# Kernel optimization log

Hardware: AMD Instinct MI355X
Metric: run time of the kernel (lower is better)

## Reference

```python
import jax, jax.numpy as jnp
import numpy as np

IN_FEATURES = 4096
OUT_FEATURES = 4096
BLOCKSIZE = 64
FP4_CODEBOOK = np.array([0.0, 0.0052, 0.6667, 1.0, 0.3333, 0.5, 0.1667, 0.25,
                         0.0, -0.0052, -0.6667, -1.0, -0.3333, -0.5, -0.1667, -0.25],
                        dtype=np.float32)


def setup_inputs() -> dict:
    key = jax.random.key(0)
    k1, k2, k3, k4 = jax.random.split(key, 4)
    n_elements = OUT_FEATURES * IN_FEATURES
    n_blocks = n_elements // BLOCKSIZE
    x = jax.random.normal(k1, (4, 2048, IN_FEATURES), dtype=jnp.float32)
    weight_packed = jax.random.randint(k2, (n_elements // 2,), 0, 256, dtype=jnp.int32)
    scale = jax.random.uniform(k3, (n_blocks,), dtype=jnp.float32)
    bias = jax.random.normal(k4, (OUT_FEATURES,), dtype=jnp.float32)
    return {"x": x, "weight_packed": weight_packed, "scale": scale, "bias": bias}


def reference(x, weight_packed, scale, bias):
    codebook = jnp.asarray(FP4_CODEBOOK, dtype=x.dtype)
    # Unpack two 4-bit indices per byte: high nibble first, then low nibble.
    high = (weight_packed >> 4) & 15
    low = weight_packed & 15
    indices = jnp.stack([high, low], axis=1).reshape(-1)  # [n_elements]
    # LUT dequant + per-block scale broadcast.
    deq = codebook[indices].reshape(-1, BLOCKSIZE) * scale[:, None]  # [n_blocks, blocksize]
    weight = deq.reshape(OUT_FEATURES, IN_FEATURES)
    # F.linear(x, W, b) = x @ W.T + b
    return jnp.einsum('bsi,oi->bso', x, weight) + bias
```

## Files before the change

kernel.cpp:

```cpp
#include <hip/hip_runtime.h>
#include <stdint.h>
#include <stddef.h>

#define IN_F 4096
#define OUT_F 4096
#define M_TOT 8192

#define BM 128
#define BN 128
#define BK 64

#define BM2 256
#define BN2 256
#define BK2 64
#define NT2 (IN_F / BK2)

typedef __attribute__((ext_vector_type(8))) short short8;
typedef __attribute__((ext_vector_type(4))) float f32x4;
typedef __attribute__((ext_vector_type(4))) float float4v;
typedef __attribute__((ext_vector_type(4))) unsigned short u16x4;
typedef __attribute__((ext_vector_type(8))) unsigned short u16x8;
typedef unsigned short u16;

__constant__ float c_lut[16] = {
  0.0f, 0.0052f, 0.6667f, 1.0f, 0.3333f, 0.5f, 0.1667f, 0.25f,
  0.0f, -0.0052f, -0.6667f, -1.0f, -0.3333f, -0.5f, -0.1667f, -0.25f
};

__device__ __forceinline__ u16 f2bf(float f) {
  unsigned int x = __float_as_uint(f);
  x += 0x7fffu + ((x >> 16) & 1u);
  return (u16)(x >> 16);
}

__device__ __forceinline__ void gload_lds16(const u16* g, u16* lds) {
  __builtin_amdgcn_global_load_lds(
      (const __attribute__((address_space(1))) unsigned int*)g,
      (__attribute__((address_space(3))) unsigned int*)lds, 16, 0, 0);
}

#define BARRIER() do { asm volatile("" ::: "memory"); \
                       __builtin_amdgcn_s_barrier();  \
                       asm volatile("" ::: "memory"); } while (0)
#define LGKM0() asm volatile("s_waitcnt lgkmcnt(0)" ::: "memory")

__global__ __launch_bounds__(256) void k_convert_x(const float* __restrict__ x,
                                                   u16* __restrict__ a) {
  const int n8 = (M_TOT * IN_F) / 8;
  const int stride = gridDim.x * blockDim.x;
  for (int t = blockIdx.x * blockDim.x + threadIdx.x; t < n8; t += stride) {
    float4v f0 = ((const float4v*)x)[2 * t];
    float4v f1 = ((const float4v*)x)[2 * t + 1];
    u16x8 o;
    o[0] = f2bf(f0.x); o[1] = f2bf(f0.y); o[2] = f2bf(f0.z); o[3] = f2bf(f0.w);
    o[4] = f2bf(f1.x); o[5] = f2bf(f1.y); o[6] = f2bf(f1.z); o[7] = f2bf(f1.w);
    ((u16x8*)a)[t] = o;
  }
}

__global__ __launch_bounds__(256) void k_dequant_w(const int* __restrict__ wp,
                                                   const float* __restrict__ scale,
                                                   u16* __restrict__ b) {
  __shared__ float lut[16];
  if (threadIdx.x < 16) lut[threadIdx.x] = c_lut[threadIdx.x];
  __syncthreads();
  const int ng = (OUT_F * IN_F / 2) / 4;
  const int stride = gridDim.x * blockDim.x;
  for (int t = blockIdx.x * blockDim.x + threadIdx.x; t < ng; t += stride) {
    int4 p = ((const int4*)wp)[t];
    float s = scale[t >> 3];
    int by[4] = {p.x, p.y, p.z, p.w};
    u16x8 o;
#pragma unroll
    for (int q = 0; q < 4; ++q) {
      o[2 * q]     = f2bf(lut[(by[q] >> 4) & 15] * s);
      o[2 * q + 1] = f2bf(lut[by[q] & 15] * s);
    }
    ((u16x8*)b)[t] = o;
  }
}


__device__ __forceinline__ void stage_a_half(const u16* __restrict__ A, u16* dst,
                                             int mBase, int kt, int h,
                                             int wave, int srow, int scol) {
#pragma unroll
  for (int n = 0; n < 2; ++n) {
    const int r0 = n * 128 + h * 64 + wave * 8;
    gload_lds16(A + (size_t)(mBase + r0 + srow) * IN_F + kt + scol, dst + r0 * BK2);
  }
}

__device__ __forceinline__ void stage_b_half(const u16* __restrict__ B, u16* dst,
                                             int nBase, int kt, int jh,
                                             int wave, int srow, int scol) {
#pragma unroll
  for (int n = 0; n < 2; ++n) {
    const int slot = wave * 2 + n;
    const int r0 = (slot >> 2) * 64 + jh * 32 + (slot & 3) * 8;
    gload_lds16(B + (size_t)(nBase + r0 + srow) * IN_F + kt + scol, dst + r0 * BK2);
  }
}

__device__ __forceinline__ void read_a4(const u16* As_c, int aBase, int co0, int co1,
                                        short8 a[4][2], int h) {
#pragma unroll
  for (int ii = 0; ii < 4; ++ii) {
    const int ro = aBase + (h * 4 + ii) * (16 * BK2);
    a[ii][0] = *(const short8*)&As_c[ro + co0];
    a[ii][1] = *(const short8*)&As_c[ro + co1];
  }
}

__device__ __forceinline__ void read_b2(const u16* Bs_c, int bBase, int co0, int co1,
                                        short8 b[2][2], int jh) {
#pragma unroll
  for (int jj = 0; jj < 2; ++jj) {
    const int ro = bBase + (jh * 2 + jj) * (16 * BK2);
    b[jj][0] = *(const short8*)&Bs_c[ro + co0];
    b[jj][1] = *(const short8*)&Bs_c[ro + co1];
  }
}

__device__ __forceinline__ void mma_quad(f32x4 acc[8][4], const short8 a[4][2],
                                         const short8 b[2][2], int h, int jh) {
#pragma unroll
  for (int k2 = 0; k2 < 2; ++k2)
#pragma unroll
    for (int ii = 0; ii < 4; ++ii)
#pragma unroll
      for (int jj = 0; jj < 2; ++jj)
        acc[h * 4 + ii][jh * 2 + jj] = __builtin_amdgcn_mfma_f32_16x16x32_bf16(
            a[ii][k2], b[jj][k2], acc[h * 4 + ii][jh * 2 + jj], 0, 0, 0);
}

__global__ __launch_bounds__(512, 2) void k_gemm256(const u16* __restrict__ A,
                                                    const u16* __restrict__ B,
                                                    const float* __restrict__ bias,
                                                    float* __restrict__ C) {
  __shared__ u16 As[2][BM2 * BK2];
  __shared__ u16 Bs[2][BN2 * BK2];

  const int tid  = threadIdx.x;
  const int lane = tid & 63;
  const int wave = tid >> 6;

  const int bid   = blockIdx.x;
  const int xcd   = bid & 7;
  const int k     = bid >> 3;
  const int tileM = (xcd >> 1) * 8 + (k >> 3);
  const int tileN = (xcd & 1) * 8 + (k & 7);
  const int mBase = tileM * BM2;
  const int nBase = tileN * BN2;

  const int wm = (wave >> 2) * 128;
  const int wn = (wave & 3) * 64;

  const int srow = lane >> 3;
  const int scol = ((lane & 7) ^ srow) * 8;

  const int frow = lane & 15;
  const int fx   = frow & 7;
  const int cq   = lane >> 4;
  const int co0  = ((cq ^ fx) << 3);
  const int co1  = (((4 + cq) ^ fx) << 3);
  const int aBase = (wm + frow) * BK2;
  const int bBase = (wn + frow) * BK2;

  f32x4 acc[8][4] = {};

  stage_a_half(A, As[0], mBase, 0, 0, wave, srow, scol);
  stage_a_half(A, As[0], mBase, 0, 1, wave, srow, scol);
  stage_b_half(B, Bs[0], nBase, 0, 0, wave, srow, scol);
  stage_b_half(B, Bs[0], nBase, 0, 1, wave, srow, scol);
  stage_a_half(A, As[1], mBase, BK2, 0, wave, srow, scol);
  stage_b_half(B, Bs[1], nBase, BK2, 1, wave, srow, scol);
  stage_a_half(A, As[1], mBase, BK2, 1, wave, srow, scol);
  asm volatile("s_waitcnt vmcnt(6)" ::: "memory");
  BARRIER();

  short8 a[4][2], b[2][2];

#pragma unroll 2
  for (int t = 0; t < NT2; ++t) {
    const int c = t & 1;
    u16* AsC = As[c];
    u16* BsC = Bs[c];
    u16* BsO = Bs[c ^ 1];
    const int kt1 = (t + 1) * BK2;
    const int kt2 = (t + 2) * BK2;

    read_a4(AsC, aBase, co0, co1, a, 0);
    read_b2(BsC, bBase, co0, co1, b, 0);
    if (t + 1 < NT2) stage_b_half(B, BsO, nBase, kt1, 0, wave, srow, scol);
    BARRIER();
    LGKM0();
    __builtin_amdgcn_s_setprio(1);
    mma_quad(acc, a, b, 0, 0);
    __builtin_amdgcn_s_setprio(0);
    BARRIER();

    read_b2(BsC, bBase, co0, co1, b, 1);
    if (t + 2 < NT2) stage_a_half(A, AsC, mBase, kt2, 0, wave, srow, scol);
    BARRIER();
    LGKM0();
    __builtin_amdgcn_s_setprio(1);
    mma_quad(acc, a, b, 0, 1);
    __builtin_amdgcn_s_setprio(0);
    BARRIER();

    read_a4(AsC, aBase, co0, co1, a, 1);
    if (t + 2 < NT2) stage_b_half(B, BsC, nBase, kt2, 1, wave, srow, scol);
    BARRIER();
    LGKM0();
    __builtin_amdgcn_s_setprio(1);
    mma_quad(acc, a, b, 1, 1);
    __builtin_amdgcn_s_setprio(0);
    BARRIER();

    read_b2(BsC, bBase, co0, co1, b, 0);
    if (t + 2 < NT2) stage_a_half(A, AsC, mBase, kt2, 1, wave, srow, scol);
    BARRIER();
    LGKM0();
    __builtin_amdgcn_s_setprio(1);
    mma_quad(acc, a, b, 1, 0);
    __builtin_amdgcn_s_setprio(0);
    if (t < NT2 - 2) asm volatile("s_waitcnt vmcnt(6)" ::: "memory");
    else             asm volatile("s_waitcnt vmcnt(0)" ::: "memory");
    BARRIER();
  }

  const int ccol = lane & 15;
  const int crow = (lane >> 4) * 4;
#pragma unroll
  for (int j = 0; j < 4; ++j) {
    const int col = nBase + wn + j * 16 + ccol;
    const float bv = bias[col];
#pragma unroll
    for (int i = 0; i < 8; ++i) {
      const size_t rb = (size_t)(mBase + wm + i * 16 + crow) * OUT_F + col;
#pragma unroll
      for (int tt = 0; tt < 4; ++tt)
        C[rb + (size_t)tt * OUT_F] = acc[i][j][tt] + bv;
    }
  }
}

__global__ __launch_bounds__(256) void k_gemm_fused(const float* __restrict__ X,
                                                    const int* __restrict__ WP,
                                                    const float* __restrict__ scale,
                                                    const float* __restrict__ bias,
                                                    float* __restrict__ C) {
  __shared__ u16 As[BM * BK];
  __shared__ u16 Bs[BN * BK];
  __shared__ float lut[16];
  const int tid = threadIdx.x;
  if (tid < 16) lut[tid] = c_lut[tid];
  const int lane = tid & 63;
  const int wave = tid >> 6;
  const int mBase = blockIdx.y * BM;
  const int nBase = blockIdx.x * BN;
  const int wm = (wave >> 1) * 64;
  const int wn = (wave & 1) * 64;
  const int frow = lane & 15;
  const int fx   = lane & 7;
  const int cq   = lane >> 4;
  f32x4 acc[4][4] = {};
  __syncthreads();

  for (int kt = 0; kt < IN_F; kt += BK) {
#pragma unroll
    for (int i = 0; i < 8; ++i) {
      const int g = tid + i * 256;
      const int r = g >> 4, c = (g & 15) * 4;
      float4v f = *(const float4v*)&X[(size_t)(mBase + r) * IN_F + kt + c];
      u16x4 o;
      o.x = f2bf(f.x); o.y = f2bf(f.y); o.z = f2bf(f.z); o.w = f2bf(f.w);
      *(u16x4*)&As[r * BK + ((((c >> 3) ^ (r & 7)) << 3) | (c & 7))] = o;
    }
#pragma unroll
    for (int i = 0; i < 4; ++i) {
      const int g = tid + i * 256;
      const int r = g >> 3, c4 = (g & 7) * 4;
      int4 p = *(const int4*)&WP[(size_t)(nBase + r) * (IN_F / 2) + (kt >> 1) + c4];
      const float s = scale[(nBase + r) * 64 + (kt >> 6)];
      int by[4] = {p.x, p.y, p.z, p.w};
      u16x8 o;
#pragma unroll
      for (int q = 0; q < 4; ++q) {
        o[2 * q]     = f2bf(lut[(by[q] >> 4) & 15] * s);
        o[2 * q + 1] = f2bf(lut[by[q] & 15] * s);
      }
      *(u16x8*)&Bs[r * BK + (((g & 7) ^ (r & 7)) << 3)] = o;
    }
    __syncthreads();
#pragma unroll
    for (int ks = 0; ks < BK; ks += 32) {
      const int co = (((ks >> 3) + cq) ^ fx) << 3;
      short8 a[4], b[4];
#pragma unroll
      for (int i = 0; i < 4; ++i)
        a[i] = *(const short8*)&As[(wm + i * 16 + frow) * BK + co];
#pragma unroll
      for (int j = 0; j < 4; ++j)
        b[j] = *(const short8*)&Bs[(wn + j * 16 + frow) * BK + co];
#pragma unroll
      for (int i = 0; i < 4; ++i)
#pragma unroll
        for (int j = 0; j < 4; ++j)
          acc[i][j] = __builtin_amdgcn_mfma_f32_16x16x32_bf16(a[i], b[j], acc[i][j], 0, 0, 0);
    }
    __syncthreads();
  }

  const int ccol = lane & 15;
  const int crow = (lane >> 4) * 4;
#pragma unroll
  for (int j = 0; j < 4; ++j) {
    const int col = nBase + wn + j * 16 + ccol;
    const float bv = bias[col];
#pragma unroll
    for (int i = 0; i < 4; ++i) {
      const size_t rb = (size_t)(mBase + wm + i * 16 + crow) * OUT_F + col;
#pragma unroll
      for (int t = 0; t < 4; ++t)
        C[rb + (size_t)t * OUT_F] = acc[i][j][t] + bv;
    }
  }
}

extern "C" void kernel_launch(void* const* d_in, const int* in_sizes, int n_in,
                              void* d_out, int out_size, void* d_ws, size_t ws_size,
                              hipStream_t stream) {
  const float* x  = (const float*)d_in[0];
  const int*   wp = (const int*)d_in[1];
  const float* sc = (const float*)d_in[2];
  const float* bi = (const float*)d_in[3];
  float* out = (float*)d_out;

  const size_t bBytes = (size_t)OUT_F * IN_F * 2;
  const size_t aBytes = (size_t)M_TOT * IN_F * 2;

  if (ws_size >= aBytes + bBytes) {
    u16* B = (u16*)d_ws;
    u16* A = (u16*)((char*)d_ws + bBytes);
    k_dequant_w<<<2048, 256, 0, stream>>>(wp, sc, B);
    k_convert_x<<<4096, 256, 0, stream>>>(x, A);
    k_gemm256<<<(M_TOT / BM2) * (OUT_F / BN2), 512, 0, stream>>>(A, B, bi, out);
  } else {
    dim3 grid(OUT_F / BN, M_TOT / BM);
    k_gemm_fused<<<grid, 256, 0, stream>>>(x, wp, sc, bi, out);
  }
}
```

Baseline: 489.0 us.

## Merge prep kernels and restructure GEMM main loop with fewer barriers

Fuses weight dequantization and x-to-bf16 conversion into one launch, splitting blocks between the two jobs. The 256x256 GEMM main loop is rescheduled into four phases: all B fragments are read once per k-tile, A is read in pairs, and global-to-LDS staging is spread across phases at finer granularity. Each phase now has one barrier instead of two, and the LDS reads for the next phase are issued right after the current MFMAs. The aim is less barrier stall and one fewer launch. In exchange the code holds more B fragments in registers, and vmcnt accounting changes, which risks races if a count is wrong.

After: 502.4 us. 2.7% more time.

```diff
diff --git a/kernel.cpp b/kernel.cpp
--- a/kernel.cpp
+++ b/kernel.cpp
@@ -44,94 +44,88 @@
                        asm volatile("" ::: "memory"); } while (0)
 #define LGKM0() asm volatile("s_waitcnt lgkmcnt(0)" ::: "memory")
 
-__global__ __launch_bounds__(256) void k_convert_x(const float* __restrict__ x,
-                                                   u16* __restrict__ a) {
-  const int n8 = (M_TOT * IN_F) / 8;
-  const int stride = gridDim.x * blockDim.x;
-  for (int t = blockIdx.x * blockDim.x + threadIdx.x; t < n8; t += stride) {
-    float4v f0 = ((const float4v*)x)[2 * t];
-    float4v f1 = ((const float4v*)x)[2 * t + 1];
-    u16x8 o;
-    o[0] = f2bf(f0.x); o[1] = f2bf(f0.y); o[2] = f2bf(f0.z); o[3] = f2bf(f0.w);
-    o[4] = f2bf(f1.x); o[5] = f2bf(f1.y); o[6] = f2bf(f1.z); o[7] = f2bf(f1.w);
-    ((u16x8*)a)[t] = o;
-  }
-}
-
-__global__ __launch_bounds__(256) void k_dequant_w(const int* __restrict__ wp,
-                                                   const float* __restrict__ scale,
-                                                   u16* __restrict__ b) {
-  __shared__ float lut[16];
-  if (threadIdx.x < 16) lut[threadIdx.x] = c_lut[threadIdx.x];
-  __syncthreads();
-  const int ng = (OUT_F * IN_F / 2) / 4;
-  const int stride = gridDim.x * blockDim.x;
-  for (int t = blockIdx.x * blockDim.x + threadIdx.x; t < ng; t += stride) {
-    int4 p = ((const int4*)wp)[t];
-    float s = scale[t >> 3];
-    int by[4] = {p.x, p.y, p.z, p.w};
-    u16x8 o;
-#pragma unroll
-    for (int q = 0; q < 4; ++q) {
-      o[2 * q]     = f2bf(lut[(by[q] >> 4) & 15] * s);
-      o[2 * q + 1] = f2bf(lut[by[q] & 15] * s);
-    }
-    ((u16x8*)b)[t] = o;
-  }
-}
-
-
-__device__ __forceinline__ void stage_a_half(const u16* __restrict__ A, u16* dst,
-                                             int mBase, int kt, int h,
-                                             int wave, int srow, int scol) {
-#pragma unroll
-  for (int n = 0; n < 2; ++n) {
-    const int r0 = n * 128 + h * 64 + wave * 8;
-    gload_lds16(A + (size_t)(mBase + r0 + srow) * IN_F + kt + scol, dst + r0 * BK2);
-  }
-}
-
-__device__ __forceinline__ void stage_b_half(const u16* __restrict__ B, u16* dst,
-                                             int nBase, int kt, int jh,
-                                             int wave, int srow, int scol) {
-#pragma unroll
-  for (int n = 0; n < 2; ++n) {
-    const int slot = wave * 2 + n;
-    const int r0 = (slot >> 2) * 64 + jh * 32 + (slot & 3) * 8;
-    gload_lds16(B + (size_t)(nBase + r0 + srow) * IN_F + kt + scol, dst + r0 * BK2);
-  }
-}
-
-__device__ __forceinline__ void read_a4(const u16* As_c, int aBase, int co0, int co1,
-                                        short8 a[4][2], int h) {
-#pragma unroll
-  for (int ii = 0; ii < 4; ++ii) {
-    const int ro = aBase + (h * 4 + ii) * (16 * BK2);
+__global__ __launch_bounds__(256) void k_prep(const float* __restrict__ x,
+                                              u16* __restrict__ a,
+                                              const int* __restrict__ wp,
+                                              const float* __restrict__ scale,
+                                              u16* __restrict__ b) {
+  if (blockIdx.x < 512) {
+    __shared__ float lut[16];
+    if (threadIdx.x < 16) lut[threadIdx.x] = c_lut[threadIdx.x];
+    __syncthreads();
+    const int ng = (OUT_F * IN_F / 2) / 4;
+    const int stride = 512 * 256;
+    for (int t = blockIdx.x * 256 + threadIdx.x; t < ng; t += stride) {
+      int4 p = ((const int4*)wp)[t];
+      float s = scale[t >> 3];
+      int by[4] = {p.x, p.y, p.z, p.w};
+      u16x8 o;
+#pragma unroll
+      for (int q = 0; q < 4; ++q) {
+        o[2 * q]     = f2bf(lut[(by[q] >> 4) & 15] * s);
+        o[2 * q + 1] = f2bf(lut[by[q] & 15] * s);
+      }
+      ((u16x8*)b)[t] = o;
+    }
+  } else {
+    const int n8 = (M_TOT * IN_F) / 8;
+    const int stride = 4096 * 256;
+    for (int t = (blockIdx.x - 512) * 256 + threadIdx.x; t < n8; t += stride) {
+      float4v f0 = ((const float4v*)x)[2 * t];
+      float4v f1 = ((const float4v*)x)[2 * t + 1];
+      u16x8 o;
+      o[0] = f2bf(f0.x); o[1] = f2bf(f0.y); o[2] = f2bf(f0.z); o[3] = f2bf(f0.w);
+      o[4] = f2bf(f1.x); o[5] = f2bf(f1.y); o[6] = f2bf(f1.z); o[7] = f2bf(f1.w);
+      ((u16x8*)a)[t] = o;
+    }
+  }
+}
+
+
+__device__ __forceinline__ void stage_b_round(const u16* __restrict__ B, u16* dst,
+                                              int nBase, int kt, int r,
+                                              int wave, int srow, int scol) {
+  const int r0 = r * 64 + wave * 8;
+  gload_lds16(B + (size_t)(nBase + r0 + srow) * IN_F + kt + scol, dst + r0 * BK2);
+}
+
+__device__ __forceinline__ void stage_a_round(const u16* __restrict__ A, u16* dst,
+                                              int mBase, int kt, int r,
+                                              int wave, int srow, int scol) {
+  const int r0 = (wave & 3) * 8 + (wave >> 2) * 128 + r * 32;
+  gload_lds16(A + (size_t)(mBase + r0 + srow) * IN_F + kt + scol, dst + r0 * BK2);
+}
+
+__device__ __forceinline__ void read_b_all(const u16* Bs_c, int bBase, int co0, int co1,
+                                           short8 b[4][2]) {
+#pragma unroll
+  for (int jj = 0; jj < 4; ++jj) {
+    const int ro = bBase + jj * (16 * BK2);
+    b[jj][0] = *(const short8*)&Bs_c[ro + co0];
+    b[jj][1] = *(const short8*)&Bs_c[ro + co1];
+  }
+}
+
+__device__ __forceinline__ void read_a_pair(const u16* As_c, int aBase, int co0, int co1,
+                                            short8 a[2][2], int p) {
+#pragma unroll
+  for (int ii = 0; ii < 2; ++ii) {
+    const int ro = aBase + (p * 2 + ii) * (16 * BK2);
     a[ii][0] = *(const short8*)&As_c[ro + co0];
     a[ii][1] = *(const short8*)&As_c[ro + co1];
   }
 }
 
-__device__ __forceinline__ void read_b2(const u16* Bs_c, int bBase, int co0, int co1,
-                                        short8 b[2][2], int jh) {
-#pragma unroll
-  for (int jj = 0; jj < 2; ++jj) {
-    const int ro = bBase + (jh * 2 + jj) * (16 * BK2);
-    b[jj][0] = *(const short8*)&Bs_c[ro + co0];
-    b[jj][1] = *(const short8*)&Bs_c[ro + co1];
-  }
-}
-
-__device__ __forceinline__ void mma_quad(f32x4 acc[8][4], const short8 a[4][2],
-                                         const short8 b[2][2], int h, int jh) {
+__device__ __forceinline__ void mma_pair(f32x4 acc[8][4], const short8 a[2][2],
+                                         const short8 b[4][2], int p) {
 #pragma unroll
   for (int k2 = 0; k2 < 2; ++k2)
 #pragma unroll
-    for (int ii = 0; ii < 4; ++ii)
-#pragma unroll
-      for (int jj = 0; jj < 2; ++jj)
-        acc[h * 4 + ii][jh * 2 + jj] = __builtin_amdgcn_mfma_f32_16x16x32_bf16(
-            a[ii][k2], b[jj][k2], acc[h * 4 + ii][jh * 2 + jj], 0, 0, 0);
+    for (int ii = 0; ii < 2; ++ii)
+#pragma unroll
+      for (int jj = 0; jj < 4; ++jj)
+        acc[p * 2 + ii][jj] = __builtin_amdgcn_mfma_f32_16x16x32_bf16(
+            a[ii][k2], b[jj][k2], acc[p * 2 + ii][jj], 0, 0, 0);
 }
 
 __global__ __launch_bounds__(512, 2) void k_gemm256(const u16* __restrict__ A,
@@ -168,67 +162,68 @@
   const int bBase = (wn + frow) * BK2;
 
   f32x4 acc[8][4] = {};
-
-  stage_a_half(A, As[0], mBase, 0, 0, wave, srow, scol);
-  stage_a_half(A, As[0], mBase, 0, 1, wave, srow, scol);
-  stage_b_half(B, Bs[0], nBase, 0, 0, wave, srow, scol);
-  stage_b_half(B, Bs[0], nBase, 0, 1, wave, srow, scol);
-  stage_a_half(A, As[1], mBase, BK2, 0, wave, srow, scol);
-  stage_b_half(B, Bs[1], nBase, BK2, 1, wave, srow, scol);
-  stage_a_half(A, As[1], mBase, BK2, 1, wave, srow, scol);
-  asm volatile("s_waitcnt vmcnt(6)" ::: "memory");
+  short8 a[2][2], b[4][2];
+
+#define SB(dst, t, r) stage_b_round(B, dst, nBase, (t) * BK2, r, wave, srow, scol)
+#define SA(dst, t, r) stage_a_round(A, dst, mBase, (t) * BK2, r, wave, srow, scol)
+
+  SB(Bs[0], 0, 0); SB(Bs[0], 0, 1); SB(Bs[0], 0, 2); SB(Bs[0], 0, 3);
+  SA(As[0], 0, 0); SA(As[0], 0, 1); SA(As[0], 0, 2); SA(As[0], 0, 3);
+  SB(Bs[1], 1, 0); SB(Bs[1], 1, 1); SA(As[1], 1, 0);
+  SB(Bs[1], 1, 2); SB(Bs[1], 1, 3); SA(As[1], 1, 1);
+  SA(As[1], 1, 2);
+  asm volatile("s_waitcnt vmcnt(7)" ::: "memory");
   BARRIER();
-
-  short8 a[4][2], b[2][2];
-
-#pragma unroll 2
+  read_b_all(Bs[0], bBase, co0, co1, b);
+  read_a_pair(As[0], aBase, co0, co1, a, 0);
+
   for (int t = 0; t < NT2; ++t) {
     const int c = t & 1;
     u16* AsC = As[c];
     u16* BsC = Bs[c];
+    u16* AsO = As[c ^ 1];
     u16* BsO = Bs[c ^ 1];
-    const int kt1 = (t + 1) * BK2;
-    const int kt2 = (t + 2) * BK2;
-
-    read_a4(AsC, aBase, co0, co1, a, 0);
-    read_b2(BsC, bBase, co0, co1, b, 0);
-    if (t + 1 < NT2) stage_b_half(B, BsO, nBase, kt1, 0, wave, srow, scol);
-    BARRIER();
+
+    if (t + 1 < NT2) SA(AsO, t + 1, 3);
     LGKM0();
     __builtin_amdgcn_s_setprio(1);
-    mma_quad(acc, a, b, 0, 0);
+    mma_pair(acc, a, b, 0);
     __builtin_amdgcn_s_setprio(0);
+    read_a_pair(AsC, aBase, co0, co1, a, 1);
     BARRIER();
 
-    read_b2(BsC, bBase, co0, co1, b, 1);
-    if (t + 2 < NT2) stage_a_half(A, AsC, mBase, kt2, 0, wave, srow, scol);
-    BARRIER();
+    if (t + 2 < NT2) { SB(BsC, t + 2, 0); SB(BsC, t + 2, 1); SA(AsC, t + 2, 0); }
     LGKM0();
     __builtin_amdgcn_s_setprio(1);
-    mma_quad(acc, a, b, 0, 1);
+    mma_pair(acc, a, b, 1);
     __builtin_amdgcn_s_setprio(0);
+    read_a_pair(AsC, aBase, co0, co1, a, 2);
     BARRIER();
 
-    read_a4(AsC, aBase, co0, co1, a, 1);
-    if (t + 2 < NT2) stage_b_half(B, BsC, nBase, kt2, 1, wave, srow, scol);
-    BARRIER();
+    if (t + 2 < NT2) { SB(BsC, t + 2, 2); SB(BsC, t + 2, 3); SA(AsC, t + 2, 1); }
     LGKM0();
     __builtin_amdgcn_s_setprio(1);
-    mma_quad(acc, a, b, 1, 1);
+    mma_pair(acc, a, b, 2);
     __builtin_amdgcn_s_setprio(0);
+    read_a_pair(AsC, aBase, co0, co1, a, 3);
     BARRIER();
 
-    read_b2(BsC, bBase, co0, co1, b, 0);
-    if (t + 2 < NT2) stage_a_half(A, AsC, mBase, kt2, 1, wave, srow, scol);
-    BARRIER();
+    if (t + 2 < NT2) SA(AsC, t + 2, 2);
     LGKM0();
     __builtin_amdgcn_s_setprio(1);
-    mma_quad(acc, a, b, 1, 0);
+    mma_pair(acc, a, b, 3);
     __builtin_amdgcn_s_setprio(0);
-    if (t < NT2 - 2) asm volatile("s_waitcnt vmcnt(6)" ::: "memory");
-    else             asm volatile("s_waitcnt vmcnt(0)" ::: "memory");
+    if (t + 1 < NT2) {
+      if (t < NT2 - 2) asm volatile("s_waitcnt vmcnt(7)" ::: "memory");
+      else             asm volatile("s_waitcnt vmcnt(0)" ::: "memory");
+      read_b_all(BsO, bBase, co0, co1, b);
+      read_a_pair(AsO, aBase, co0, co1, a, 0);
+    }
     BARRIER();
   }
+
+#undef SB
+#undef SA
 
   const int ccol = lane & 15;
   const int crow = (lane >> 4) * 4;
@@ -344,8 +339,7 @@
   if (ws_size >= aBytes + bBytes) {
     u16* B = (u16*)d_ws;
     u16* A = (u16*)((char*)d_ws + bBytes);
-    k_dequant_w<<<2048, 256, 0, stream>>>(wp, sc, B);
-    k_convert_x<<<4096, 256, 0, stream>>>(x, A);
+    k_prep<<<4608, 256, 0, stream>>>(x, A, wp, sc, B);
     k_gemm256<<<(M_TOT / BM2) * (OUT_F / BN2), 512, 0, stream>>>(A, B, bi, out);
   } else {
     dim3 grid(OUT_F / BN, M_TOT / BM);
```
